# Kernel tuning notes

Measured on AMD Instinct MI355X. Metric: run time of the kernel, lower is better.

The kernel has to match this reference:

```python
import jax, jax.numpy as jnp
import numpy as np

B, L = 2, 1024
D_MODEL, D_STATE, HEADDIM, EXPAND = 512, 16, 64, 2
D_INNER = EXPAND * D_MODEL          # 1024
NHEADS = D_INNER // HEADDIM         # 16
DCONV = 4
NLAYERS = 6
FFN = 4 * D_MODEL                   # 2048
CONV_DIM = D_INNER + 2 * D_STATE    # 1056
D_IN_PROJ = 2 * D_INNER + 2 * D_STATE + NHEADS  # 2096


def _rms(x, w, eps):
    return x * jax.lax.rsqrt(jnp.mean(x * x, axis=-1, keepdims=True) + eps) * w


def _mamba2(u, W_in, conv_w, conv_b, A_log, Dh, dt_bias, norm_w, W_out):
    # u: (b, l, d_model). Standard Mamba2 block (ngroups=1).
    b, l, _ = u.shape
    zxbcdt = u @ W_in                                   # (b, l, D_IN_PROJ)
    z = zxbcdt[..., :D_INNER]
    xBC = zxbcdt[..., D_INNER:D_INNER + CONV_DIM]
    dt = jax.nn.softplus(zxbcdt[..., D_INNER + CONV_DIM:] + dt_bias)  # (b, l, h)
    # causal depthwise conv, kernel size DCONV
    xpad = jnp.pad(xBC, ((0, 0), (DCONV - 1, 0), (0, 0)))
    xconv = conv_b + sum(xpad[:, k:k + l, :] * conv_w[:, k] for k in range(DCONV))
    xBC = jax.nn.silu(xconv)
    xh = xBC[..., :D_INNER].reshape(b, l, NHEADS, HEADDIM)
    Bm = xBC[..., D_INNER:D_INNER + D_STATE]            # (b, l, n)
    Cm = xBC[..., D_INNER + D_STATE:]                   # (b, l, n)
    A = -jnp.exp(A_log)                                 # (h,)
    dA = jnp.exp(dt * A)                                # (b, l, h)
    dtx = dt[..., None] * xh                            # (b, l, h, p)

    def step(h, inp):
        dA_t, dtx_t, B_t, C_t = inp
        h = h * dA_t[:, :, None, None] + dtx_t[..., None] * B_t[:, None, None, :]
        y = jnp.einsum('bhpn,bn->bhp', h, C_t)
        return h, y

    xs = (jnp.moveaxis(dA, 1, 0), jnp.moveaxis(dtx, 1, 0),
          jnp.moveaxis(Bm, 1, 0), jnp.moveaxis(Cm, 1, 0))
    h0 = jnp.zeros((b, NHEADS, HEADDIM, D_STATE), u.dtype)
    _, ys = jax.lax.scan(step, h0, xs)                  # (l, b, h, p)
    y = jnp.moveaxis(ys, 0, 1) + Dh[None, None, :, None] * xh
    y = y.reshape(b, l, D_INNER) * jax.nn.silu(z)       # gated
    y = _rms(y, norm_w, 1e-5)
    return y @ W_out


def _forward(x, position_embedding, pixel_mask, W_in, conv_w, conv_b, A_log, D,
             dt_bias, mnorm_w, W_out, norm_ssm_w, ffn_w1, ffn_b1, ffn_w2, ffn_b2,
             norm_ffn_w, final_norm_w):
    mask = pixel_mask[..., None]
    for i in range(NLAYERS):
        h = _rms(x, norm_ssm_w[i], 1e-6)
        s = (h + position_embedding) * mask
        fwd = _mamba2(s, W_in[i, 0], conv_w[i, 0], conv_b[i, 0], A_log[i, 0],
                      D[i, 0], dt_bias[i, 0], mnorm_w[i, 0], W_out[i, 0])
        bwd = jnp.flip(_mamba2(jnp.flip(s, 1), W_in[i, 1], conv_w[i, 1], conv_b[i, 1],
                               A_log[i, 1], D[i, 1], dt_bias[i, 1], mnorm_w[i, 1],
                               W_out[i, 1]), 1)
        x = x + 0.5 * (fwd + bwd) * mask
        hf = _rms(x, norm_ffn_w[i], 1e-6)
        x = x + jax.nn.gelu(hf @ ffn_w1[i] + ffn_b1[i], approximate=False) @ ffn_w2[i] + ffn_b2[i]
    return _rms(x, final_norm_w, 1e-6)


def setup_inputs() -> dict:
    key = jax.random.key(0)
    ks = jax.random.split(key, 12)
    s = 0.02
    f32 = jnp.float32
    return {
        'x': jax.random.normal(ks[0], (B, L, D_MODEL), f32),
        'position_embedding': jax.random.normal(ks[1], (B, L, D_MODEL), f32),
        'pixel_mask': jnp.ones((B, L), f32),
        'W_in': s * jax.random.normal(ks[2], (NLAYERS, 2, D_MODEL, D_IN_PROJ), f32),
        'conv_w': 0.3 * jax.random.normal(ks[3], (NLAYERS, 2, CONV_DIM, DCONV), f32),
        'conv_b': jnp.zeros((NLAYERS, 2, CONV_DIM), f32),
        'A_log': jnp.log(jax.random.uniform(ks[4], (NLAYERS, 2, NHEADS), f32, 1.0, 16.0)),
        'D': jnp.ones((NLAYERS, 2, NHEADS), f32),
        'dt_bias': jax.random.uniform(ks[5], (NLAYERS, 2, NHEADS), f32, -4.0, -1.0),
        'mnorm_w': jnp.ones((NLAYERS, 2, D_INNER), f32),
        'W_out': s * jax.random.normal(ks[6], (NLAYERS, 2, D_INNER, D_MODEL), f32),
        'norm_ssm_w': jnp.ones((NLAYERS, D_MODEL), f32),
        'ffn_w1': s * jax.random.normal(ks[7], (NLAYERS, D_MODEL, FFN), f32),
        'ffn_b1': jnp.zeros((NLAYERS, FFN), f32),
        'ffn_w2': s * jax.random.normal(ks[8], (NLAYERS, FFN, D_MODEL), f32),
        'ffn_b2': jnp.zeros((NLAYERS, D_MODEL), f32),
        'norm_ffn_w': jnp.ones((NLAYERS, D_MODEL), f32),
        'final_norm_w': jnp.ones((D_MODEL,), f32),
    }


def reference(x, position_embedding, pixel_mask, W_in, conv_w, conv_b, A_log, D,
              dt_bias, mnorm_w, W_out, norm_ssm_w, ffn_w1, ffn_b1, ffn_w2, ffn_b2,
              norm_ffn_w, final_norm_w):
    return _forward(x, position_embedding, pixel_mask, W_in, conv_w, conv_b, A_log, D,
                    dt_bias, mnorm_w, W_out, norm_ssm_w, ffn_w1, ffn_b1, ffn_w2, ffn_b2,
                    norm_ffn_w, final_norm_w)
```

## Files before the change

### kernel.cpp

```cpp
#include <hip/hip_runtime.h>
#include <cstdint>
#include <cstddef>

typedef __bf16 bf16;
typedef __bf16 bf16x4 __attribute__((ext_vector_type(4)));
typedef __bf16 bf16x8 __attribute__((ext_vector_type(8)));
typedef float f32x4 __attribute__((ext_vector_type(4)));

#define L_SEQ   1024
#define DMODEL  512
#define DINNER  1024
#define DSTATE  16
#define NHEADS  16
#define HEADDIM 64
#define CONVDIM 1056
#define DINPROJ 2096
#define FFN_DIM 2048
#define ROWS    2048
#define CHUNK   64
#define NCHUNK  16
#define SLAB    ((size_t)ROWS * DMODEL)

__device__ __forceinline__ float wave_sum(float v) {
#pragma unroll
  for (int off = 32; off; off >>= 1) v += __shfl_down(v, off, 64);
  return v;
}
__device__ __forceinline__ float silu_f(float x) { return x / (1.0f + expf(-x)); }

__global__ __launch_bounds__(128) void rms_kernel(
    const float* __restrict__ x, const float* __restrict__ w,
    const float* __restrict__ pe, const float* __restrict__ mask,
    bf16* __restrict__ outb)
{
  int r = blockIdx.x, t = threadIdx.x;
  float4 v = ((const float4*)(x + (size_t)r * DMODEL))[t];
  float ss = v.x*v.x + v.y*v.y + v.z*v.z + v.w*v.w;
  ss = wave_sum(ss);
  __shared__ float red[2];
  if ((t & 63) == 0) red[t >> 6] = ss;
  __syncthreads();
  float rs = 1.0f / sqrtf((red[0] + red[1]) * (1.0f / DMODEL) + 1e-6f);
  float4 wv = ((const float4*)w)[t];
  float4 p = ((const float4*)(pe + (size_t)r * DMODEL))[t];
  float m = mask[r];
  bf16x4 o;
  o[0] = (bf16)((v.x*rs*wv.x + p.x) * m);
  o[1] = (bf16)((v.y*rs*wv.y + p.y) * m);
  o[2] = (bf16)((v.z*rs*wv.z + p.z) * m);
  o[3] = (bf16)((v.w*rs*wv.w + p.w) * m);
  *(bf16x4*)&outb[(size_t)r * DMODEL + t * 4] = o;
}

__global__ __launch_bounds__(256) void transpose_all(
    const float* __restrict__ W_in, const float* __restrict__ W_out,
    const float* __restrict__ f1, const float* __restrict__ f2,
    bf16* __restrict__ TIN, bf16* __restrict__ TOUT,
    bf16* __restrict__ T1, bf16* __restrict__ T2)
{
  int bid = blockIdx.x;
  const float* src; bf16* dst; int K, N, k0, n0;
  if (bid < 3168) {
    int slice = bid / 264, rem = bid % 264;
    K = 512; N = 2096;
    k0 = (rem & 3) * 128; n0 = (rem >> 2) * 32;
    src = W_in + (size_t)slice * K * N;  dst = TIN + (size_t)slice * N * K;
  } else if (bid < 4704) {
    int t2 = bid - 3168;
    int slice = t2 / 128, rem = t2 % 128;
    K = 1024; N = 512;
    k0 = (rem & 7) * 128; n0 = (rem >> 3) * 32;
    src = W_out + (size_t)slice * K * N; dst = TOUT + (size_t)slice * N * K;
  } else if (bid < 6240) {
    int t3 = bid - 4704;
    int slice = t3 / 256, rem = t3 % 256;
    K = 512; N = 2048;
    k0 = (rem & 3) * 128; n0 = (rem >> 2) * 32;
    src = f1 + (size_t)slice * K * N;    dst = T1 + (size_t)slice * N * K;
  } else {
    int t4 = bid - 6240;
    int slice = t4 / 256, rem = t4 % 256;
    K = 2048; N = 512;
    k0 = (rem & 15) * 128; n0 = (rem >> 4) * 32;
    src = f2 + (size_t)slice * K * N;    dst = T2 + (size_t)slice * N * K;
  }
  __shared__ float tile[128][33];
  int fq = threadIdx.x & 7, kr = threadIdx.x >> 3;
#pragma unroll
  for (int p = 0; p < 4; p++) {
    int k = kr + 32 * p;
    float4 v = {0.0f, 0.0f, 0.0f, 0.0f};
    int n = n0 + fq * 4;
    if (n < N) v = *(const float4*)&src[(size_t)(k0 + k) * N + n];
    int cq = (fq * 4) ^ (((k >> 3) & 7) << 2);
    *(float4*)&tile[k][cq] = v;
  }
  __syncthreads();
  int kg = threadIdx.x & 15, nb = threadIdx.x >> 4;
#pragma unroll
  for (int p = 0; p < 2; p++) {
    int nn = nb + 16 * p;
    if (n0 + nn < N) {
      bf16x8 o;
#pragma unroll
      for (int j = 0; j < 8; j++) {
        int row = kg * 8 + j;
        o[j] = (bf16)tile[row][nn ^ (((row >> 3) & 7) << 2)];
      }
      *(bf16x8*)&dst[(size_t)(n0 + nn) * K + k0 + kg * 8] = o;
    }
  }
}

template<int BM, int BN, int FI, int FJ, int MODE>
__global__ __launch_bounds__(256) void gemm_tile(
    const bf16* __restrict__ A, const bf16* __restrict__ BT,
    float* __restrict__ Cf, bf16* __restrict__ Cb,
    int M, int N, int K, int lda, int ldb,
    long aOffz, long bOffz, long cOffz, int flipz, int kspl,
    const float* __restrict__ bias)
{
  constexpr int CH = (BM + BN) * 8;
  constexpr int NI = CH / 256;
  constexpr int HC = CH / 2;
  constexpr int HALF = (BM + BN) * 32;

  int z = blockIdx.z;
  int dir = z / kspl, ks = z - dir * kspl;
  A  += (size_t)dir * aOffz + (size_t)ks * K;
  BT += (size_t)dir * bOffz + (size_t)ks * K;
  long coff = (size_t)z * cOffz;
  int doflip = (flipz && dir == 1);

  __shared__ __align__(16) bf16 Tile[2 * HALF];

  int m0 = blockIdx.x * BM, n0 = blockIdx.y * BN;
  int t = threadIdx.x;
  int lane = t & 63, w = t >> 6;
  int wr = w >> 1, wc = w & 1;
  int lr = lane & 15, lq = lane >> 4;

  const bf16* gsrc[NI];
  int ldsoff[NI];
#pragma unroll
  for (int i = 0; i < NI; i++) {
    int g0 = w * (CH / 4) + i * 64;
    int g  = g0 + lane;
    int half = g / HC;
    int wi = g - half * HC;
    int row = wi >> 2, kp = wi & 3;
    int kcol = half * 32 + kp * 8;
    if (row < BM) {
      int gr = m0 + row;
      if (doflip) gr ^= (L_SEQ - 1);
      gsrc[i] = A + (size_t)gr * lda + kcol;
    } else {
      int gn = n0 + (row - BM); if (gn >= N) gn = N - 1;
      gsrc[i] = BT + (size_t)gn * ldb + kcol;
    }
    int half0 = g0 / HC, wi0 = g0 - half0 * HC;
    ldsoff[i] = half0 * HALF + wi0 * 8;
  }

  f32x4 zf = {0.0f, 0.0f, 0.0f, 0.0f};
  f32x4 acc[FI][FJ];
#pragma unroll
  for (int i = 0; i < FI; i++)
#pragma unroll
    for (int j = 0; j < FJ; j++) acc[i][j] = zf;

  for (int k0 = 0; k0 < K; k0 += 64) {
#pragma unroll
    for (int i = 0; i < NI; i++) {
      __builtin_amdgcn_global_load_lds(
          (const __attribute__((address_space(1))) void*)(gsrc[i] + k0),
          (__attribute__((address_space(3))) void*)&Tile[ldsoff[i]],
          16, 0, 0);
    }
    __syncthreads();

#pragma unroll
    for (int hf = 0; hf < 2; hf++) {
      const bf16* As = Tile + hf * HALF;
      const bf16* Bs = As + BM * 32;
      bf16x8 af[FI], bfv[FJ];
#pragma unroll
      for (int i = 0; i < FI; i++)
        af[i] = *(const bf16x8*)&As[(wr * 64 + i * 16 + lr) * 32 + lq * 8];
#pragma unroll
      for (int j = 0; j < FJ; j++)
        bfv[j] = *(const bf16x8*)&Bs[(wc * (BN / 2) + j * 16 + lr) * 32 + lq * 8];
#pragma unroll
      for (int i = 0; i < FI; i++)
#pragma unroll
        for (int j = 0; j < FJ; j++)
          acc[i][j] = __builtin_amdgcn_mfma_f32_16x16x32_bf16(af[i], bfv[j], acc[i][j], 0, 0, 0);
    }
    __syncthreads();
  }

#pragma unroll
  for (int i = 0; i < FI; i++) {
    int growb = m0 + wr * 64 + i * 16 + lq * 4;
#pragma unroll
    for (int j = 0; j < FJ; j++) {
      int gcol = n0 + wc * (BN / 2) + j * 16 + lr;
      if (gcol >= N) continue;
#pragma unroll
      for (int rr = 0; rr < 4; rr++) {
        int grow = growb + rr;
        float v = acc[i][j][rr];
        if (MODE == 1) {
          v += bias[gcol];
          v = 0.5f * v * (1.0f + erff(v * 0.70710678118f));
          Cb[coff + (size_t)grow * N + gcol] = (bf16)v;
        } else if (MODE == 3) {
          Cb[coff + (size_t)grow * N + gcol] = (bf16)v;
          if (gcol >= DINNER + CONVDIM)
            Cf[(size_t)z * ROWS * 16 + (size_t)grow * 16 + (gcol - (DINNER + CONVDIM))] = v;
        } else {
          Cf[coff + (size_t)grow * N + gcol] = v;
        }
      }
    }
  }
}

__global__ __launch_bounds__(64) void convdt_bc(
    const bf16* __restrict__ ZX, const float* __restrict__ DTRAW,
    float* __restrict__ BCf, float* __restrict__ DT, float* __restrict__ DA,
    const float* __restrict__ conv_w, const float* __restrict__ conv_b,
    const float* __restrict__ dt_bias, const float* __restrict__ A_log)
{
  int r = blockIdx.x, dir = blockIdx.y;
  int l = r & (L_SEQ - 1);
  int t = threadIdx.x;
  if (t < 32) {
    int ch = DINNER + t;
    const float* cw = conv_w + ((size_t)dir * CONVDIM + ch) * 4;
    float acc = conv_b[(size_t)dir * CONVDIM + ch];
    const bf16* zc = ZX + (size_t)dir * ROWS * DINPROJ + DINNER + ch;
#pragma unroll
    for (int k = 0; k < 4; k++) {
      int ls = l + k - 3;
      if (ls >= 0) acc += (float)zc[(size_t)(r + k - 3) * DINPROJ] * cw[k];
    }
    BCf[((size_t)dir * ROWS + r) * 32 + t] = silu_f(acc);
  } else if (t < 48) {
    int h = t - 32;
    float raw = DTRAW[((size_t)dir * ROWS + r) * 16 + h] + dt_bias[dir * NHEADS + h];
    float dt = (raw > 20.0f) ? raw : log1pf(expf(raw));
    float A = -expf(A_log[dir * NHEADS + h]);
    size_t idx = ((size_t)dir * ROWS + r) * NHEADS + h;
    DT[idx] = dt;
    DA[idx] = expf(dt * A);
  }
}

__global__ __launch_bounds__(64) void scan1_kernel(
    const bf16* __restrict__ ZX, const float* __restrict__ BCf,
    const float* __restrict__ DT, const float* __restrict__ DA,
    bf16* __restrict__ YSSM, float* __restrict__ HEND,
    float* __restrict__ APROD,
    const float* __restrict__ conv_w, const float* __restrict__ conv_b,
    const float* __restrict__ Dparam)
{
  int bid = blockIdx.x;
  int g = bid >> 4, c = bid & 15;
  int dir = g >> 5, rem = g & 31;
  int b = rem >> 4, h = rem & 15;
  int lane = threadIdx.x;
  size_t rowbase = (size_t)dir * ROWS + b * L_SEQ + c * CHUNK;

  float dtv = DT[(rowbase + lane) * NHEADS + h];
  float dav = DA[(rowbase + lane) * NHEADS + h];

  float ap = dav;
#pragma unroll
  for (int off = 1; off < 64; off <<= 1) {
    float o = __shfl_up(ap, off, 64);
    if (lane >= off) ap *= o;
  }
  APROD[((size_t)g * NCHUNK + c) * 64 + lane] = ap;

  __shared__ float BCs[CHUNK][36];
#pragma unroll
  for (int i = 0; i < 8; i++) {
    int l = i * 8 + (lane >> 3), f = lane & 7;
    float4 v = *(const float4*)&BCf[(rowbase + l) * 32 + f * 4];
    *(float4*)&BCs[l][f * 4] = v;
  }
  __syncthreads();

  int ch = h * HEADDIM + lane;
  f32x4 cwv = *(const f32x4*)&conv_w[((size_t)dir * CONVDIM + ch) * 4];
  float cbv = conv_b[(size_t)dir * CONVDIM + ch];
  const bf16* xcol = ZX + rowbase * DINPROJ + DINNER + ch;
  int lg0 = c * CHUNK;
  float xm3 = (lg0 >= 3) ? (float)xcol[-3 * DINPROJ] : 0.0f;
  float xm2 = (lg0 >= 2) ? (float)xcol[-2 * DINPROJ] : 0.0f;
  float xm1 = (lg0 >= 1) ? (float)xcol[-1 * DINPROJ] : 0.0f;

  float Dv = Dparam[dir * NHEADS + h];

  float hs[16];
#pragma unroll
  for (int n = 0; n < 16; n++) hs[n] = 0.0f;

  bf16* yp = YSSM + rowbase * DINNER + ch;

#pragma unroll 4
  for (int l = 0; l < CHUNK; l++) {
    float dt = __shfl(dtv, l, 64);
    float da = __shfl(dav, l, 64);
    float xcur = (float)xcol[(size_t)l * DINPROJ];
    float conv = cbv + cwv[0]*xm3 + cwv[1]*xm2 + cwv[2]*xm1 + cwv[3]*xcur;
    xm3 = xm2; xm2 = xm1; xm1 = xcur;
    float xv = silu_f(conv);
    float4 bq[4], cq[4];
#pragma unroll
    for (int q = 0; q < 4; q++) {
      bq[q] = *(const float4*)&BCs[l][q * 4];
      cq[q] = *(const float4*)&BCs[l][16 + q * 4];
    }
    const float* Bv = (const float*)bq;
    const float* Cv = (const float*)cq;
    float dtx = dt * xv;
    float acc = 0.0f;
#pragma unroll
    for (int n = 0; n < 16; n++) {
      hs[n] = hs[n] * da + dtx * Bv[n];
      acc += hs[n] * Cv[n];
    }
    yp[(size_t)l * DINNER] = (bf16)(acc + Dv * xv);
  }

  float* he = HEND + ((size_t)g * NCHUNK + c) * 16 * 64;
#pragma unroll
  for (int n = 0; n < 16; n++) he[n * 64 + lane] = hs[n];
}

__global__ __launch_bounds__(64) void scan2_kernel(
    const float* __restrict__ BCf, bf16* __restrict__ YSSM,
    const float* __restrict__ HEND, const float* __restrict__ APROD)
{
  int bid = blockIdx.x;
  int g = bid >> 4, c = bid & 15;
  if (c == 0) return;
  int dir = g >> 5, rem = g & 31;
  int b = rem >> 4, h = rem & 15;
  int lane = threadIdx.x;

  float hstart[16];
#pragma unroll
  for (int n = 0; n < 16; n++) hstart[n] = 0.0f;
  float w = 1.0f;
  for (int j = c - 1; j >= 0; j--) {
    const float* he = HEND + ((size_t)g * NCHUNK + j) * 16 * 64;
#pragma unroll
    for (int n = 0; n < 16; n++) hstart[n] += w * he[n * 64 + lane];
    w *= APROD[((size_t)g * NCHUNK + j) * 64 + 63];
  }

  size_t rowbase = (size_t)dir * ROWS + b * L_SEQ + c * CHUNK;
  bf16* yp = YSSM + rowbase * DINNER + h * HEADDIM + lane;
  float apv = APROD[((size_t)g * NCHUNK + c) * 64 + lane];

  __shared__ float Cs[CHUNK][20];
#pragma unroll
  for (int i = 0; i < 4; i++) {
    int l = i * 16 + (lane >> 2), f = lane & 3;
    float4 v = *(const float4*)&BCf[(rowbase + l) * 32 + 16 + f * 4];
    *(float4*)&Cs[l][f * 4] = v;
  }
  __syncthreads();

#pragma unroll 4
  for (int l = 0; l < CHUNK; l++) {
    float a = __shfl(apv, l, 64);
    float4 cq[4];
#pragma unroll
    for (int q = 0; q < 4; q++) cq[q] = *(const float4*)&Cs[l][q * 4];
    const float* Cv = (const float*)cq;
    float acc = 0.0f;
#pragma unroll
    for (int n = 0; n < 16; n++) acc += Cv[n] * hstart[n];
    float y = (float)yp[(size_t)l * DINNER];
    yp[(size_t)l * DINNER] = (bf16)(y + a * acc);
  }
}

__global__ __launch_bounds__(256) void gatenorm_kernel(
    const bf16* __restrict__ YSSM, const bf16* __restrict__ ZX,
    const float* __restrict__ mnorm_w, bf16* __restrict__ YB)
{
  int r = blockIdx.x, dir = blockIdx.y, t = threadIdx.x;
  const bf16* y = YSSM + ((size_t)dir * ROWS + r) * DINNER;
  const bf16* z  = ZX  + ((size_t)dir * ROWS + r) * DINPROJ;
  int c = t * 4;
  bf16x4 yv4 = *(const bf16x4*)&y[c];
  bf16x4 zv4 = *(const bf16x4*)&z[c];
  float val[4];
#pragma unroll
  for (int q = 0; q < 4; q++)
    val[q] = (float)yv4[q] * silu_f((float)zv4[q]);
  float ss = val[0]*val[0] + val[1]*val[1] + val[2]*val[2] + val[3]*val[3];
  ss = wave_sum(ss);
  __shared__ float red[4];
  if ((t & 63) == 0) red[t >> 6] = ss;
  __syncthreads();
  float total = red[0] + red[1] + red[2] + red[3];
  float rs = 1.0f / sqrtf(total * (1.0f / DINNER) + 1e-5f);
  float4 wv = *(const float4*)&mnorm_w[dir * DINNER + c];
  bf16x4 o;
  o[0] = (bf16)(val[0] * rs * wv.x);
  o[1] = (bf16)(val[1] * rs * wv.y);
  o[2] = (bf16)(val[2] * rs * wv.z);
  o[3] = (bf16)(val[3] * rs * wv.w);
  *(bf16x4*)&YB[((size_t)dir * ROWS + r) * DINNER + c] = o;
}

__global__ __launch_bounds__(128) void combine_rms(
    const float* __restrict__ Xsrc, float* __restrict__ X,
    const float* __restrict__ P, const float* __restrict__ mask,
    const float* __restrict__ w, bf16* __restrict__ outb)
{
  int r = blockIdx.x, t = threadIdx.x;
  int b = r >> 10, l = r & 1023;
  int c = t * 4;
  float m = 0.5f * mask[r];
  float4 f0 = *(const float4*)&P[(size_t)r * DMODEL + c];
  float4 f1 = *(const float4*)&P[SLAB + (size_t)r * DMODEL + c];
  size_t fr = (size_t)(b * L_SEQ + (L_SEQ - 1 - l)) * DMODEL + c;
  float4 b0 = *(const float4*)&P[2 * SLAB + fr];
  float4 b1 = *(const float4*)&P[3 * SLAB + fr];
  float4 x = *(const float4*)&Xsrc[(size_t)r * DMODEL + c];
  x.x += m * (f0.x + f1.x + b0.x + b1.x);
  x.y += m * (f0.y + f1.y + b0.y + b1.y);
  x.z += m * (f0.z + f1.z + b0.z + b1.z);
  x.w += m * (f0.w + f1.w + b0.w + b1.w);
  *(float4*)&X[(size_t)r * DMODEL + c] = x;
  float ss = x.x*x.x + x.y*x.y + x.z*x.z + x.w*x.w;
  ss = wave_sum(ss);
  __shared__ float red[2];
  if ((t & 63) == 0) red[t >> 6] = ss;
  __syncthreads();
  float rs = 1.0f / sqrtf((red[0] + red[1]) * (1.0f / DMODEL) + 1e-6f);
  float4 wv = *(const float4*)&w[c];
  bf16x4 o;
  o[0] = (bf16)(x.x * rs * wv.x);
  o[1] = (bf16)(x.y * rs * wv.y);
  o[2] = (bf16)(x.z * rs * wv.z);
  o[3] = (bf16)(x.w * rs * wv.w);
  *(bf16x4*)&outb[(size_t)r * DMODEL + c] = o;
}

__global__ __launch_bounds__(128) void reduce_rms(
    float* __restrict__ X, const float* __restrict__ P,
    const float* __restrict__ bias, const float* __restrict__ w,
    const float* __restrict__ pe, const float* __restrict__ mask,
    bf16* __restrict__ outb, float* __restrict__ outf)
{
  int r = blockIdx.x, t = threadIdx.x;
  int c = t * 4;
  size_t off = (size_t)r * DMODEL + c;
  float4 a0 = *(const float4*)&P[off];
  float4 a1 = *(const float4*)&P[SLAB + off];
  float4 a2 = *(const float4*)&P[2 * SLAB + off];
  float4 a3 = *(const float4*)&P[3 * SLAB + off];
  float4 bi = *(const float4*)&bias[c];
  float4 x  = *(float4*)&X[off];
  x.x += a0.x + a1.x + a2.x + a3.x + bi.x;
  x.y += a0.y + a1.y + a2.y + a3.y + bi.y;
  x.z += a0.z + a1.z + a2.z + a3.z + bi.z;
  x.w += a0.w + a1.w + a2.w + a3.w + bi.w;
  *(float4*)&X[off] = x;
  float ss = x.x*x.x + x.y*x.y + x.z*x.z + x.w*x.w;
  ss = wave_sum(ss);
  __shared__ float red[2];
  if ((t & 63) == 0) red[t >> 6] = ss;
  __syncthreads();
  float rs = 1.0f / sqrtf((red[0] + red[1]) * (1.0f / DMODEL) + 1e-6f);
  float4 wv = *(const float4*)&w[c];
  float4 o;
  o.x = x.x*rs*wv.x; o.y = x.y*rs*wv.y; o.z = x.z*rs*wv.z; o.w = x.w*rs*wv.w;
  if (pe) {
    float4 p = *(const float4*)&pe[off];
    float m = mask[r];
    o.x = (o.x + p.x)*m; o.y = (o.y + p.y)*m; o.z = (o.z + p.z)*m; o.w = (o.w + p.w)*m;
  }
  if (outb) {
    bf16x4 ob = {(bf16)o.x, (bf16)o.y, (bf16)o.z, (bf16)o.w};
    *(bf16x4*)&outb[off] = ob;
  } else {
    *(float4*)&outf[off] = o;
  }
}

extern "C" void kernel_launch(void* const* d_in, const int* in_sizes, int n_in,
                              void* d_out, int out_size, void* d_ws, size_t ws_size,
                              hipStream_t stream)
{
  const float* in_x    = (const float*)d_in[0];
  const float* in_pe   = (const float*)d_in[1];
  const float* in_mask = (const float*)d_in[2];
  const float* W_in    = (const float*)d_in[3];
  const float* conv_w  = (const float*)d_in[4];
  const float* conv_b  = (const float*)d_in[5];
  const float* A_log   = (const float*)d_in[6];
  const float* Dparam  = (const float*)d_in[7];
  const float* dt_bias = (const float*)d_in[8];
  const float* mnorm_w = (const float*)d_in[9];
  const float* W_out   = (const float*)d_in[10];
  const float* nssm_w  = (const float*)d_in[11];
  const float* ffn_w1  = (const float*)d_in[12];
  const float* ffn_b1  = (const float*)d_in[13];
  const float* ffn_w2  = (const float*)d_in[14];
  const float* ffn_b2  = (const float*)d_in[15];
  const float* nffn_w  = (const float*)d_in[16];
  const float* final_w = (const float*)d_in[17];

  if (ws_size < 126287872) return;

  char* ws = (char*)d_ws;
  float* XBUF  = (float*)(ws + 0);
  bf16*  SBUF  = (bf16*) (ws + 4194304);
  bf16*  ZXb   = (bf16*) (ws + 6291456);
  float* DOUTf = (float*)(ws + 6291456);
  float* DTRAW = (float*)(ws + 23461888);
  float* BCf   = (float*)(ws + 23724032);
  float* DTb   = (float*)(ws + 24248320);
  float* DAb   = (float*)(ws + 24510464);
  bf16*  YSSMb = (bf16*) (ws + 24772608);
  bf16*  YB    = (bf16*) (ws + 33161216);
  bf16*  MID   = (bf16*) (ws + 41549824);
  float* HEND  = (float*)(ws + 49938432);
  float* APROD = (float*)(ws + 54132736);
  bf16*  WTINa = (bf16*) (ws + 62783488);
  bf16*  WTOUTa= (bf16*) (ws + 88539136);
  bf16*  WT1a  = (bf16*) (ws + 101122048);
  bf16*  WT2a  = (bf16*) (ws + 113704960);

  transpose_all<<<7776, 256, 0, stream>>>(W_in, W_out, ffn_w1, ffn_w2,
                                          WTINa, WTOUTa, WT1a, WT2a);
  rms_kernel<<<ROWS, 128, 0, stream>>>(in_x, nssm_w, in_pe, in_mask, SBUF);

  for (int layer = 0; layer < 6; layer++) {
    const bf16* WTIN  = WTINa  + (size_t)layer * 2 * DMODEL * DINPROJ;
    const bf16* WTOUT = WTOUTa + (size_t)layer * 2 * DINNER * DMODEL;
    const bf16* WT1   = WT1a   + (size_t)layer * DMODEL * FFN_DIM;
    const bf16* WT2   = WT2a   + (size_t)layer * FFN_DIM * DMODEL;
    const float* cw_l = conv_w + (size_t)layer * 2 * CONVDIM * 4;
    const float* cb_l = conv_b + (size_t)layer * 2 * CONVDIM;

    gemm_tile<128, 128, 4, 4, 3><<<dim3(16, 17, 2), 256, 0, stream>>>(
        SBUF, WTIN, DTRAW, ZXb, ROWS, DINPROJ, DMODEL, DMODEL, DMODEL,
        0L, (long)DINPROJ * DMODEL, (long)ROWS * DINPROJ, 1, 1, nullptr);
    convdt_bc<<<dim3(ROWS, 2), 64, 0, stream>>>(
        ZXb, DTRAW, BCf, DTb, DAb, cw_l, cb_l,
        dt_bias + layer * 2 * NHEADS, A_log + layer * 2 * NHEADS);
    scan1_kernel<<<1024, 64, 0, stream>>>(
        ZXb, BCf, DTb, DAb, YSSMb, HEND, APROD, cw_l, cb_l,
        Dparam + layer * 2 * NHEADS);
    scan2_kernel<<<1024, 64, 0, stream>>>(BCf, YSSMb, HEND, APROD);
    gatenorm_kernel<<<dim3(ROWS, 2), 256, 0, stream>>>(
        YSSMb, ZXb, mnorm_w + layer * 2 * DINNER, YB);
    gemm_tile<128, 64, 4, 2, 0><<<dim3(16, 8, 4), 256, 0, stream>>>(
        YB, WTOUT, DOUTf, nullptr, ROWS, DMODEL, 512, DINNER, DINNER,
        (long)ROWS * DINNER, (long)DMODEL * DINNER, (long)SLAB, 0, 2, nullptr);
    combine_rms<<<ROWS, 128, 0, stream>>>(
        layer == 0 ? in_x : XBUF, XBUF, DOUTf, in_mask, nffn_w + layer * DMODEL, SBUF);

    gemm_tile<128, 64, 4, 2, 1><<<dim3(16, 32, 1), 256, 0, stream>>>(
        SBUF, WT1, nullptr, MID, ROWS, FFN_DIM, DMODEL, DMODEL, DMODEL,
        0L, 0L, 0L, 0, 1, ffn_b1 + layer * FFN_DIM);
    gemm_tile<128, 64, 4, 2, 0><<<dim3(16, 8, 4), 256, 0, stream>>>(
        MID, WT2, DOUTf, nullptr, ROWS, DMODEL, 512, FFN_DIM, FFN_DIM,
        0L, 0L, (long)SLAB, 0, 4, nullptr);
    if (layer < 5) {
      reduce_rms<<<ROWS, 128, 0, stream>>>(
          XBUF, DOUTf, ffn_b2 + layer * DMODEL, nssm_w + (layer + 1) * DMODEL,
          in_pe, in_mask, SBUF, nullptr);
    } else {
      reduce_rms<<<ROWS, 128, 0, stream>>>(
          XBUF, DOUTf, ffn_b2 + layer * DMODEL, final_w,
          nullptr, nullptr, nullptr, (float*)d_out);
    }
  }
}
```

Measured before the change: 950.1 us.

## Fuse conv/dt preprocessing into scan kernels and drop convdt_bc

Removes the separate convdt_bc kernel and its intermediate BCf/DT/DA buffers. scan1 now computes softplus(dt) and exp(dt*A) inline, and runs the causal conv plus SiLU for the B and C channels straight from ZX into shared memory. scan2 recomputes the conv for the C channels itself. This saves one launch per layer and a round trip through global memory. In exchange, every head block redundantly recomputes the same B/C conv with a serial, latency-bound loop of strided bf16 loads.

```diff
diff --git a/kernel.cpp b/kernel.cpp
--- a/kernel.cpp
+++ b/kernel.cpp
@@ -226,43 +226,12 @@
   }
 }
 
-__global__ __launch_bounds__(64) void convdt_bc(
+__global__ __launch_bounds__(64) void scan1_kernel(
     const bf16* __restrict__ ZX, const float* __restrict__ DTRAW,
-    float* __restrict__ BCf, float* __restrict__ DT, float* __restrict__ DA,
-    const float* __restrict__ conv_w, const float* __restrict__ conv_b,
-    const float* __restrict__ dt_bias, const float* __restrict__ A_log)
-{
-  int r = blockIdx.x, dir = blockIdx.y;
-  int l = r & (L_SEQ - 1);
-  int t = threadIdx.x;
-  if (t < 32) {
-    int ch = DINNER + t;
-    const float* cw = conv_w + ((size_t)dir * CONVDIM + ch) * 4;
-    float acc = conv_b[(size_t)dir * CONVDIM + ch];
-    const bf16* zc = ZX + (size_t)dir * ROWS * DINPROJ + DINNER + ch;
-#pragma unroll
-    for (int k = 0; k < 4; k++) {
-      int ls = l + k - 3;
-      if (ls >= 0) acc += (float)zc[(size_t)(r + k - 3) * DINPROJ] * cw[k];
-    }
-    BCf[((size_t)dir * ROWS + r) * 32 + t] = silu_f(acc);
-  } else if (t < 48) {
-    int h = t - 32;
-    float raw = DTRAW[((size_t)dir * ROWS + r) * 16 + h] + dt_bias[dir * NHEADS + h];
-    float dt = (raw > 20.0f) ? raw : log1pf(expf(raw));
-    float A = -expf(A_log[dir * NHEADS + h]);
-    size_t idx = ((size_t)dir * ROWS + r) * NHEADS + h;
-    DT[idx] = dt;
-    DA[idx] = expf(dt * A);
-  }
-}
-
-__global__ __launch_bounds__(64) void scan1_kernel(
-    const bf16* __restrict__ ZX, const float* __restrict__ BCf,
-    const float* __restrict__ DT, const float* __restrict__ DA,
     bf16* __restrict__ YSSM, float* __restrict__ HEND,
     float* __restrict__ APROD,
     const float* __restrict__ conv_w, const float* __restrict__ conv_b,
+    const float* __restrict__ dt_bias, const float* __restrict__ A_log,
     const float* __restrict__ Dparam)
 {
   int bid = blockIdx.x;
@@ -272,8 +241,9 @@
   int lane = threadIdx.x;
   size_t rowbase = (size_t)dir * ROWS + b * L_SEQ + c * CHUNK;
 
-  float dtv = DT[(rowbase + lane) * NHEADS + h];
-  float dav = DA[(rowbase + lane) * NHEADS + h];
+  float raw = DTRAW[(rowbase + lane) * NHEADS + h] + dt_bias[dir * NHEADS + h];
+  float dtv = (raw > 20.0f) ? raw : log1pf(expf(raw));
+  float dav = expf(dtv * (-expf(A_log[dir * NHEADS + h])));
 
   float ap = dav;
 #pragma unroll
@@ -284,11 +254,24 @@
   APROD[((size_t)g * NCHUNK + c) * 64 + lane] = ap;
 
   __shared__ float BCs[CHUNK][36];
-#pragma unroll
-  for (int i = 0; i < 8; i++) {
-    int l = i * 8 + (lane >> 3), f = lane & 7;
-    float4 v = *(const float4*)&BCf[(rowbase + l) * 32 + f * 4];
-    *(float4*)&BCs[l][f * 4] = v;
+  {
+    int cch = lane & 31;
+    int rg  = lane >> 5;
+    int r0  = rg * 32;
+    const bf16* bcol = ZX + (rowbase + r0) * DINPROJ + 2 * DINNER + cch;
+    f32x4 cw2 = *(const f32x4*)&conv_w[((size_t)dir * CONVDIM + DINNER + cch) * 4];
+    float cb2 = conv_b[(size_t)dir * CONVDIM + DINNER + cch];
+    int p0 = c * CHUNK + r0;
+    float m3 = (p0 >= 3) ? (float)bcol[-3 * DINPROJ] : 0.0f;
+    float m2 = (p0 >= 2) ? (float)bcol[-2 * DINPROJ] : 0.0f;
+    float m1 = (p0 >= 1) ? (float)bcol[-1 * DINPROJ] : 0.0f;
+#pragma unroll 4
+    for (int rr = 0; rr < 32; rr++) {
+      float xc = (float)bcol[(size_t)rr * DINPROJ];
+      float cv = cb2 + cw2[0]*m3 + cw2[1]*m2 + cw2[2]*m1 + cw2[3]*xc;
+      m3 = m2; m2 = m1; m1 = xc;
+      BCs[r0 + rr][cch] = silu_f(cv);
+    }
   }
   __syncthreads();
 
@@ -341,8 +324,9 @@
 }
 
 __global__ __launch_bounds__(64) void scan2_kernel(
-    const float* __restrict__ BCf, bf16* __restrict__ YSSM,
-    const float* __restrict__ HEND, const float* __restrict__ APROD)
+    const bf16* __restrict__ ZX, bf16* __restrict__ YSSM,
+    const float* __restrict__ HEND, const float* __restrict__ APROD,
+    const float* __restrict__ conv_w, const float* __restrict__ conv_b)
 {
   int bid = blockIdx.x;
   int g = bid >> 4, c = bid & 15;
@@ -350,6 +334,27 @@
   int dir = g >> 5, rem = g & 31;
   int b = rem >> 4, h = rem & 15;
   int lane = threadIdx.x;
+  size_t rowbase = (size_t)dir * ROWS + b * L_SEQ + c * CHUNK;
+
+  __shared__ float Cs[CHUNK][20];
+  {
+    int cch = lane & 15;
+    int rg  = lane >> 4;
+    int r0  = rg * 16;
+    const bf16* ccol = ZX + (rowbase + r0) * DINPROJ + 2 * DINNER + 16 + cch;
+    f32x4 cw2 = *(const f32x4*)&conv_w[((size_t)dir * CONVDIM + DINNER + 16 + cch) * 4];
+    float cb2 = conv_b[(size_t)dir * CONVDIM + DINNER + 16 + cch];
+    float m3 = (float)ccol[-3 * DINPROJ];
+    float m2 = (float)ccol[-2 * DINPROJ];
+    float m1 = (float)ccol[-1 * DINPROJ];
+#pragma unroll 4
+    for (int rr = 0; rr < 16; rr++) {
+      float xc = (float)ccol[(size_t)rr * DINPROJ];
+      float cv = cb2 + cw2[0]*m3 + cw2[1]*m2 + cw2[2]*m1 + cw2[3]*xc;
+      m3 = m2; m2 = m1; m1 = xc;
+      Cs[r0 + rr][cch] = silu_f(cv);
+    }
+  }
 
   float hstart[16];
 #pragma unroll
@@ -362,17 +367,8 @@
     w *= APROD[((size_t)g * NCHUNK + j) * 64 + 63];
   }
 
-  size_t rowbase = (size_t)dir * ROWS + b * L_SEQ + c * CHUNK;
   bf16* yp = YSSM + rowbase * DINNER + h * HEADDIM + lane;
   float apv = APROD[((size_t)g * NCHUNK + c) * 64 + lane];
-
-  __shared__ float Cs[CHUNK][20];
-#pragma unroll
-  for (int i = 0; i < 4; i++) {
-    int l = i * 16 + (lane >> 2), f = lane & 3;
-    float4 v = *(const float4*)&BCf[(rowbase + l) * 32 + 16 + f * 4];
-    *(float4*)&Cs[l][f * 4] = v;
-  }
   __syncthreads();
 
 #pragma unroll 4
@@ -528,9 +524,6 @@
   bf16*  ZXb   = (bf16*) (ws + 6291456);
   float* DOUTf = (float*)(ws + 6291456);
   float* DTRAW = (float*)(ws + 23461888);
-  float* BCf   = (float*)(ws + 23724032);
-  float* DTb   = (float*)(ws + 24248320);
-  float* DAb   = (float*)(ws + 24510464);
   bf16*  YSSMb = (bf16*) (ws + 24772608);
   bf16*  YB    = (bf16*) (ws + 33161216);
   bf16*  MID   = (bf16*) (ws + 41549824);
@@ -556,13 +549,11 @@
     gemm_tile<128, 128, 4, 4, 3><<<dim3(16, 17, 2), 256, 0, stream>>>(
         SBUF, WTIN, DTRAW, ZXb, ROWS, DINPROJ, DMODEL, DMODEL, DMODEL,
         0L, (long)DINPROJ * DMODEL, (long)ROWS * DINPROJ, 1, 1, nullptr);
-    convdt_bc<<<dim3(ROWS, 2), 64, 0, stream>>>(
-        ZXb, DTRAW, BCf, DTb, DAb, cw_l, cb_l,
-        dt_bias + layer * 2 * NHEADS, A_log + layer * 2 * NHEADS);
     scan1_kernel<<<1024, 64, 0, stream>>>(
-        ZXb, BCf, DTb, DAb, YSSMb, HEND, APROD, cw_l, cb_l,
+        ZXb, DTRAW, YSSMb, HEND, APROD, cw_l, cb_l,
+        dt_bias + layer * 2 * NHEADS, A_log + layer * 2 * NHEADS,
         Dparam + layer * 2 * NHEADS);
-    scan2_kernel<<<1024, 64, 0, stream>>>(BCf, YSSMb, HEND, APROD);
+    scan2_kernel<<<1024, 64, 0, stream>>>(ZXb, YSSMb, HEND, APROD, cw_l, cb_l);
     gatenorm_kernel<<<dim3(ROWS, 2), 256, 0, stream>>>(
         YSSMb, ZXb, mnorm_w + layer * 2 * DINNER, YB);
     gemm_tile<128, 64, 4, 2, 0><<<dim3(16, 8, 4), 256, 0, stream>>>(
```

Measured after the change: 990.6 us. 1.04x slower.
